# Optimization experiments

Hardware: AMD Instinct MI355X
Metric: run time of the kernel (lower is better)

Reference implementation:

```python
import jax, jax.numpy as jnp
import numpy as np

N_NODES, N_EDGES, N_GRAPHS, N_LOCS = 50000, 800000, 64, 50
HEADS, OUT_PER_HEAD = 3, 43            # ceil(128/3) = 43
MID = HEADS * OUT_PER_HEAD             # 129
GAT_HIDDEN, MLP_HIDDEN = 128, 256
NEG_SLOPE = 0.2


def _leaky(v):
    return jnp.where(v > 0, v, NEG_SLOPE * v)


def _gat_layer(h_in, src, dst, W, a_src, a_dst, b, concat):
    """PyG GATConv: per-edge attention, segment softmax over dst, scatter-add."""
    N = h_in.shape[0]
    H, O = a_src.shape
    h = (h_in @ W).reshape(N, H, O)                      # [N,H,O]
    es = jnp.einsum('nho,ho->nh', h, a_src)              # alpha_src per node
    ed = jnp.einsum('nho,ho->nh', h, a_dst)              # alpha_dst per node
    e = _leaky(es[src] + ed[dst])                        # [E,H]
    m = jax.ops.segment_max(e, dst, num_segments=N)
    m = jnp.where(jnp.isfinite(m), m, 0.0)
    w = jnp.exp(e - m[dst])
    z = jax.ops.segment_sum(w, dst, num_segments=N)
    alpha = w / (z[dst] + 1e-16)                         # softmax over in-edges of dst
    out = jax.ops.segment_sum(h[src] * alpha[:, :, None], dst, num_segments=N)
    out = out.reshape(N, H * O) if concat else out.mean(axis=1)
    return out + b


def setup_inputs() -> dict:
    key = jax.random.key(0)
    ks = jax.random.split(key, 20)
    x = jax.random.normal(ks[0], (N_NODES, 6), jnp.float32)
    edge_index = jax.random.randint(ks[1], (2, N_EDGES), 0, N_NODES)
    batch = jnp.sort(jax.random.randint(ks[2], (N_NODES,), 0, N_GRAPHS))
    loc = jax.random.uniform(ks[3], (N_GRAPHS, N_LOCS, 2), jnp.float32)

    def p(k, shape):
        return jax.random.normal(k, shape, jnp.float32) * 0.1

    return dict(
        x=x, loc=loc, edge_index=edge_index, batch=batch,
        W0=p(ks[4], (6, MID)), as0=p(ks[5], (HEADS, OUT_PER_HEAD)),
        ad0=p(ks[6], (HEADS, OUT_PER_HEAD)), b0=jnp.zeros((MID,), jnp.float32),
        W1=p(ks[7], (MID, MID)), as1=p(ks[8], (HEADS, OUT_PER_HEAD)),
        ad1=p(ks[9], (HEADS, OUT_PER_HEAD)), b1=jnp.zeros((MID,), jnp.float32),
        W2=p(ks[10], (MID, GAT_HIDDEN)), as2=p(ks[11], (1, GAT_HIDDEN)),
        ad2=p(ks[12], (1, GAT_HIDDEN)), b2=jnp.zeros((GAT_HIDDEN,), jnp.float32),
        Wl1=p(ks[13], (2, MLP_HIDDEN)), bl1=jnp.zeros((MLP_HIDDEN,), jnp.float32),
        Wl2=p(ks[14], (MLP_HIDDEN, GAT_HIDDEN)), bl2=jnp.zeros((GAT_HIDDEN,), jnp.float32),
    )


def reference(x, loc, W0, as0, ad0, b0, W1, as1, ad1, b1, W2, as2, ad2, b2,
              Wl1, bl1, Wl2, bl2, edge_index, batch):
    N = x.shape[0]
    loops = jnp.arange(N)                                # add_self_loops=True
    src = jnp.concatenate([edge_index[0], loops])
    dst = jnp.concatenate([edge_index[1], loops])

    h = _leaky(_gat_layer(x, src, dst, W0, as0, ad0, b0, True))
    h = _leaky(_gat_layer(h, src, dst, W1, as1, ad1, b1, True))
    h = _gat_layer(h, src, dst, W2, as2, ad2, b2, False)  # heads=1, concat=False

    # global_mean_pool over graphs
    sums = jax.ops.segment_sum(h, batch, num_segments=N_GRAPHS)
    cnt = jax.ops.segment_sum(jnp.ones((N, 1), h.dtype), batch, num_segments=N_GRAPHS)
    graph_emb = sums / jnp.maximum(cnt, 1.0)              # [B,128]

    # location encoder MLP + mean pool over locations
    loc_emb = jnp.tanh(loc @ Wl1 + bl1) @ Wl2 + bl2       # [B,L,128]
    loc_pooled = loc_emb.mean(axis=1)                     # [B,128]

    return jnp.concatenate([graph_emb, loc_pooled], axis=-1)  # [B,256]
```

## Files before the change

### kernel.cpp

```cpp
#include <hip/hip_runtime.h>
#include <hip/hip_bf16.h>
#include <math.h>

#define N_NODES  50000
#define N_EDGES  800000
#define E_TOT    850000
#define N_GRAPHS 64
#define N_LOCS   50
#define SCAN_B   ((N_NODES + 255) / 256)
#define TSTRIDE  128
#define HSTRIDE  132
#define ASTRIDE  160

#define EB_B     ((E_TOT + 255) / 256)
#define GEMM0_B  ((N_NODES + 31) / 32)
#define NPB3     85
#define RST3     136
#define ESED3_B  ((N_NODES + NPB3 - 1) / NPB3)
#define POOL_B   ((N_NODES + 31) / 32)

typedef __hip_bfloat16 bf16;
typedef __attribute__((ext_vector_type(8))) short bf16x8;
typedef __attribute__((ext_vector_type(4))) float f32x4;

__device__ int      g_deg[N_NODES];
__device__ int      g_rowptr[N_NODES + 1];
__device__ int      g_bsum[SCAN_B];
__device__ int      g_slot[E_TOT];
__device__ int      g_csrc[E_TOT];
__device__ float    g_Wp0[6 * 132];
__device__ __align__(256) unsigned short g_Tb[(size_t)N_NODES * TSTRIDE];
__device__ float    g_Te[N_NODES];
__device__ __align__(16) float g_H[(size_t)N_NODES * HSTRIDE];
__device__ __align__(16) unsigned short g_Ah[(size_t)N_NODES * ASTRIDE];
__device__ __align__(16) unsigned short g_Al[(size_t)N_NODES * ASTRIDE];
#define WQ1_N (5 * 9 * 64 * 8)
#define WQ2_N (5 * 8 * 64 * 8)
__device__ __align__(16) unsigned short g_Wq1h[WQ1_N], g_Wq1l[WQ1_N];
__device__ __align__(16) unsigned short g_Wq2h[WQ2_N], g_Wq2l[WQ2_N];
__device__ float    g_es[N_NODES * 3];
__device__ float    g_ed[N_NODES * 3];
__device__ unsigned g_gmk[9];
__device__ float    g_gsum[N_GRAPHS * 128];
__device__ float    g_gcnt[N_GRAPHS];

__device__ __forceinline__ float lrelu(float x){ return x > 0.f ? x : 0.2f * x; }
__device__ __forceinline__ int   clampi(int v, int lo, int hi){ return v < lo ? lo : (v > hi ? hi : v); }
__device__ __forceinline__ float finz(float v){
    unsigned u = __float_as_uint(v);
    return ((u & 0x7F800000u) == 0x7F800000u) ? 0.f : v;
}
__device__ __forceinline__ unsigned short f2bu(float x){
    union { bf16 b; unsigned short u; } cv; cv.b = __float2bfloat16(x); return cv.u;
}
__device__ __forceinline__ float bu2f(unsigned short u){ return __uint_as_float(((unsigned)u) << 16); }
__device__ __forceinline__ unsigned fkey(float f){
    unsigned u = __float_as_uint(f);
    return (u & 0x80000000u) ? ~u : (u | 0x80000000u);
}
__device__ __forceinline__ float kinv(unsigned k){
    return __uint_as_float((k & 0x80000000u) ? (k ^ 0x80000000u) : ~k);
}
__device__ __forceinline__ float expc(float a){ return __expf(fminf(fmaxf(a, -80.f), 0.f)); }
__device__ __forceinline__ void edge_sd(const int* ei, int e, int& src, int& dst){
    if (e < N_EDGES){
        src = clampi(ei[e], 0, N_NODES - 1);
        dst = clampi(ei[N_EDGES + e], 0, N_NODES - 1);
    } else {
        src = dst = e - N_EDGES;
    }
}
#define RL_I(v, i) __builtin_amdgcn_readlane((v), (i))
#define RL_F(v, i) __uint_as_float((unsigned)__builtin_amdgcn_readlane((int)__float_as_uint(v), (i)))

#define PRE_TOT (N_NODES + N_GRAPHS*128 + 9 + 6*132 + WQ1_N + WQ2_N)
__global__ void k_pre(const float* __restrict__ W0, const float* __restrict__ W1,
                      const float* __restrict__ W2){
    int i = blockIdx.x * blockDim.x + threadIdx.x;
    if (i < N_NODES){ g_deg[i] = 0; return; }
    i -= N_NODES;
    if (i < N_GRAPHS * 128){ g_gsum[i] = 0.f; return; }
    i -= N_GRAPHS * 128;
    if (i < 9){ g_gmk[i] = 0u; return; }
    i -= 9;
    if (i < 6 * 132){
        int k = i / 132, c = i - k * 132;
        g_Wp0[i] = (c < 129) ? finz(W0[k * 129 + c]) : 0.f;
        return;
    }
    i -= 6 * 132;
    if (i < WQ1_N){
        int kt = i / 4608;
        int r1 = i - kt * 4608;
        int nt = r1 / 512;
        int r2 = r1 - nt * 512;
        int ln = r2 >> 3, j = r2 & 7;
        int k = kt * 32 + (ln >> 4) * 8 + j;
        int c = nt * 16 + (ln & 15);
        float v = (k < 129 && c < 129) ? finz(W1[k * 129 + c]) : 0.f;
        unsigned short h = f2bu(v);
        g_Wq1h[i] = h;
        g_Wq1l[i] = f2bu(v - bu2f(h));
        return;
    }
    i -= WQ1_N;
    if (i < WQ2_N){
        int kt = i / 4096;
        int r1 = i - kt * 4096;
        int nt = r1 / 512;
        int r2 = r1 - nt * 512;
        int ln = r2 >> 3, j = r2 & 7;
        int k = kt * 32 + (ln >> 4) * 8 + j;
        int c = nt * 16 + (ln & 15);
        float v = (k < 129 && c < 128) ? finz(W2[k * 128 + c]) : 0.f;
        unsigned short h = f2bu(v);
        g_Wq2h[i] = h;
        g_Wq2l[i] = f2bu(v - bu2f(h));
    }
}

__global__ __launch_bounds__(256)
void k_g0deg(const float* __restrict__ X, const int* __restrict__ ei){
    if (blockIdx.x < EB_B){
        int e = blockIdx.x * 256 + threadIdx.x;
        if (e >= E_TOT) return;
        int src, dst; edge_sd(ei, e, src, dst);
        (void)src;
        g_slot[e] = atomicAdd(&g_deg[dst], 1);
        return;
    }
    const int R = 4, CO = 129;
    const float* Wp = g_Wp0;
    int bid = blockIdx.x - EB_B;
    int tid = threadIdx.x;
    int rg = tid >> 5;
    int g  = tid & 31;
    int n0 = bid * (8 * R) + rg * R;
    const float4* wp = (const float4*)Wp;
    float4 acc[R];
    float accE[R];
    #pragma unroll
    for (int r = 0; r < R; r++){ acc[r] = make_float4(0.f,0.f,0.f,0.f); accE[r] = 0.f; }

    const float* ar[R];
    #pragma unroll
    for (int r = 0; r < R; r++){
        int n = n0 + r;
        ar[r] = X + (size_t)(n < N_NODES ? n : N_NODES - 1) * 6;
    }
    #pragma unroll
    for (int k = 0; k < 6; k++){
        float4 w = wp[k * 33 + g];
        float we = (g == 0) ? Wp[k * 132 + 128] : 0.f;
        #pragma unroll
        for (int r = 0; r < R; r++){
            float a = ar[r][k];
            acc[r].x += a * w.x; acc[r].y += a * w.y;
            acc[r].z += a * w.z; acc[r].w += a * w.w;
            if (g == 0) accE[r] += a * we;
        }
    }

    #pragma unroll
    for (int r = 0; r < R; r++){
        int n = n0 + r;
        if (n >= N_NODES) break;
        unsigned* tw = (unsigned*)(g_Tb + (size_t)n * TSTRIDE);
        tw[g * 2]     = ((unsigned)f2bu(finz(acc[r].x)) ) | ((unsigned)f2bu(finz(acc[r].y)) << 16);
        tw[g * 2 + 1] = ((unsigned)f2bu(finz(acc[r].z)) ) | ((unsigned)f2bu(finz(acc[r].w)) << 16);
        if (CO > 128 && g == 0) g_Te[n] = finz(accE[r]);
    }
}

__global__ void k_scan1(){
    __shared__ int s[256];
    int i = blockIdx.x * 256 + threadIdx.x;
    int v = (i < N_NODES) ? g_deg[i] : 0;
    s[threadIdx.x] = v;
    __syncthreads();
    for (int off = 1; off < 256; off <<= 1){
        int add = (threadIdx.x >= off) ? s[threadIdx.x - off] : 0;
        __syncthreads();
        s[threadIdx.x] += add;
        __syncthreads();
    }
    if (threadIdx.x == 255) g_bsum[blockIdx.x] = s[255];
    if (i < N_NODES) g_rowptr[i] = s[threadIdx.x] - v;
}

__global__ __launch_bounds__(256)
void k_scan23(){
    __shared__ int red[256];
    int b = blockIdx.x, tid = threadIdx.x;
    red[tid] = (tid < b) ? g_bsum[tid] : 0;
    __syncthreads();
    #pragma unroll
    for (int off = 128; off >= 1; off >>= 1){
        if (tid < off) red[tid] += red[tid + off];
        __syncthreads();
    }
    int S = red[0];
    int i = b * 256 + tid;
    if (i < N_NODES) g_rowptr[i] += S;
    if (b == 0 && tid == 0) g_rowptr[N_NODES] = E_TOT;
}

__device__ __forceinline__ void esed3_body(const float* __restrict__ as,
                                           const float* __restrict__ ad,
                                           int base, int bid){
    __shared__ unsigned short rows[NPB3 * RST3];
    __shared__ unsigned sm[3];
    int tid = threadIdx.x;
    if (tid < 3) sm[tid] = 0u;
    int n0 = bid * NPB3;
    for (int ch = tid; ch < NPB3 * 16; ch += 256){
        int r = ch >> 4, k = ch & 15;
        int n = n0 + r; if (n >= N_NODES) n = N_NODES - 1;
        *(uint4*)&rows[r * RST3 + k * 8] =
            *(const uint4*)(g_Tb + (size_t)n * TSTRIDE + k * 8);
    }
    __syncthreads();
    int idx = n0 * 3 + tid;
    if (tid < NPB3 * 3 && idx < N_NODES * 3){
        int r = tid / 3, h = tid - r * 3;
        const unsigned short* rw = rows + r * RST3;
        float a = 0.f, b = 0.f;
        #pragma unroll 4
        for (int o = 0; o < 43; o++){
            int col = h * 43 + o;
            float v = (col < 128) ? bu2f(rw[col]) : finz(g_Te[n0 + r]);
            a += v * finz(as[h * 43 + o]);
            b += v * finz(ad[h * 43 + o]);
        }
        a = finz(a); b = finz(b);
        g_es[idx] = a; g_ed[idx] = b;
        atomicMax(&sm[h], fkey(a));
    }
    __syncthreads();
    if (tid < 3) atomicMax(&g_gmk[base + tid], sm[tid]);
}

__global__ __launch_bounds__(256)
void k_esed3(const float* __restrict__ as, const float* __restrict__ ad, int base){
    esed3_body(as, ad, base, blockIdx.x);
}

__global__ __launch_bounds__(256)
void k_esfill(const float* __restrict__ as, const float* __restrict__ ad,
              const int* __restrict__ ei){
    if (blockIdx.x < EB_B){
        int e = blockIdx.x * 256 + threadIdx.x;
        if (e >= E_TOT) return;
        int src, dst; edge_sd(ei, e, src, dst);
        int pos = clampi(g_rowptr[dst] + g_slot[e], 0, E_TOT - 1);
        g_csrc[pos] = src;
        return;
    }
    esed3_body(as, ad, 0, blockIdx.x - EB_B);
}

__global__ __launch_bounds__(256)
void k_esedR(const float* __restrict__ as, const float* __restrict__ ad, int base){
    __shared__ unsigned sm[1];
    int tid = threadIdx.x;
    if (tid == 0) sm[0] = 0u;
    __syncthreads();
    int n = blockIdx.x * 256 + tid;
    bool act = n < N_NODES;
    int nn = act ? n : N_NODES - 1;
    const uint4* rp = (const uint4*)(g_Tb + (size_t)nn * TSTRIDE);
    float a = 0.f, b = 0.f;
    #pragma unroll
    for (int k = 0; k < 16; k++){
        uint4 ch = rp[k];
        unsigned dw[4] = {ch.x, ch.y, ch.z, ch.w};
        #pragma unroll
        for (int j = 0; j < 4; j++){
            unsigned d = dw[j];
            int o = k * 8 + j * 2;
            float v0 = bu2f((unsigned short)(d & 0xFFFFu));
            float v1 = bu2f((unsigned short)(d >> 16));
            a += v0 * finz(as[o]);     b += v0 * finz(ad[o]);
            a += v1 * finz(as[o + 1]); b += v1 * finz(ad[o + 1]);
        }
    }
    if (act){
        a = finz(a); b = finz(b);
        g_es[n] = a; g_ed[n] = b;
        atomicMax(&sm[0], fkey(a));
    }
    __syncthreads();
    if (tid == 0) atomicMax(&g_gmk[base], sm[0]);
}

template<int NT, bool HASE>
__global__ __launch_bounds__(256, 3)
void k_gmm(){
    const unsigned short* Wh = HASE ? g_Wq1h : g_Wq2h;
    const unsigned short* Wl = HASE ? g_Wq1l : g_Wq2l;
    int lane = threadIdx.x & 63, wv = threadIdx.x >> 6;
    int row0 = blockIdx.x * 64 + wv * 16;
    int rl = row0 + (lane & 15);
    if (rl >= N_NODES) rl = N_NODES - 1;
    const bf16x8* Ah = (const bf16x8*)(g_Ah + (size_t)rl * ASTRIDE);
    const bf16x8* Al = (const bf16x8*)(g_Al + (size_t)rl * ASTRIDE);
    int ao = lane >> 4;

    f32x4 acc[NT] = {};
    #pragma unroll
    for (int kt = 0; kt < 5; kt++){
        bf16x8 ah = Ah[kt * 4 + ao];
        bf16x8 al = Al[kt * 4 + ao];
        const bf16x8* wh = (const bf16x8*)Wh + (size_t)(kt * NT) * 64 + lane;
        const bf16x8* wl = (const bf16x8*)Wl + (size_t)(kt * NT) * 64 + lane;
        #pragma unroll
        for (int t = 0; t < NT; t++){
            bf16x8 bh = wh[t * 64];
            bf16x8 bl = wl[t * 64];
            acc[t] = __builtin_amdgcn_mfma_f32_16x16x32_bf16(ah, bh, acc[t], 0, 0, 0);
            acc[t] = __builtin_amdgcn_mfma_f32_16x16x32_bf16(al, bh, acc[t], 0, 0, 0);
            acc[t] = __builtin_amdgcn_mfma_f32_16x16x32_bf16(ah, bl, acc[t], 0, 0, 0);
        }
    }

    int rq = row0 + (lane >> 4) * 4;
    int c  = lane & 15;
    #pragma unroll
    for (int t = 0; t < NT; t++){
        int col = t * 16 + c;
        #pragma unroll
        for (int q = 0; q < 4; q++){
            int rr = rq + q;
            if (rr >= N_NODES) continue;
            float v = finz(acc[t][q]);
            if (col < 128)            g_Tb[(size_t)rr * TSTRIDE + col] = f2bu(v);
            else if (HASE && col == 128) g_Te[rr] = v;
        }
    }
}

template<int H, int O, int C, bool LEAKY, bool WRITEA>
__global__ __launch_bounds__(256)
void k_fgat(const float* __restrict__ bias, int base){
    const int CH = 64 / H;
    __shared__ float lw[4][64];
    int wv = threadIdx.x >> 6, lane = threadIdx.x & 63;
    int n = blockIdx.x * 4 + wv;
    if (n >= N_NODES) return;
    int r0 = clampi(g_rowptr[n], 0, E_TOT);
    int r1 = clampi(g_rowptr[n + 1], r0, E_TOT);

    const int jmine = lane / H;
    const int hmine = lane - jmine * H;
    const float edm = finz(g_ed[n * H + hmine]);
    const float mxm = lrelu(finz(kinv(g_gmk[base + hmine])) + edm);
    const unsigned* tb = (const unsigned*)g_Tb;

    const int c0 = 2 * lane, c1 = 2 * lane + 1;
    const int h0 = c0 / O, h1 = c1 / O;
    float* lwp = lw[wv];

    float a0 = 0.f, a1 = 0.f, zA = 0.f, zB = 0.f, A2 = 0.f, z2 = 0.f;

#define EDGE(tt, pv, ss) { \
    float x0 = __uint_as_float((pv) << 16); \
    float x1 = __uint_as_float((pv) & 0xFFFF0000u); \
    float wA = lwp[(tt) * H + h0]; \
    a0 += wA * x0; zA += wA; \
    if (H > 1){ \
        float wB = lwp[(tt) * H + h1]; \
        a1 += wB * x1; zB += wB; \
    } else { \
        a1 += wA * x1; \
    } \
    if (C > 128){ \
        float w2 = lwp[(tt) * H + (H - 1)]; \
        float te = finz(g_Te[ss]); \
        A2 += w2 * te; z2 += w2; \
    } \
}

    for (int bse = r0; bse < r1; bse += CH){
        int m = r1 - bse; if (m > CH) m = CH;
        float w = 0.f; int sA = 0;
        if (jmine < m){
            sA = clampi(g_csrc[bse + jmine], 0, N_NODES - 1);
            w = expc(lrelu(finz(g_es[sA * H + hmine]) + edm) - mxm);
        }
        lwp[lane] = w;
        int t = 0;
        for (; t + 4 <= m; t += 4){
            int s0 = RL_I(sA, (t + 0) * H);
            int s1 = RL_I(sA, (t + 1) * H);
            int s2 = RL_I(sA, (t + 2) * H);
            int s3 = RL_I(sA, (t + 3) * H);
            unsigned pv0 = tb[(size_t)s0 * 64 + lane];
            unsigned pv1 = tb[(size_t)s1 * 64 + lane];
            unsigned pv2 = tb[(size_t)s2 * 64 + lane];
            unsigned pv3 = tb[(size_t)s3 * 64 + lane];
            EDGE(t + 0, pv0, s0)
            EDGE(t + 1, pv1, s1)
            EDGE(t + 2, pv2, s2)
            EDGE(t + 3, pv3, s3)
        }
        for (; t < m; ++t){
            int s0 = RL_I(sA, t * H);
            unsigned pv0 = tb[(size_t)s0 * 64 + lane];
            EDGE(t, pv0, s0)
        }
    }
#undef EDGE

    if (H == 1){ zB = zA; }

    float o0 = finz(a0 / (zA + 1e-16f)) + finz(bias[c0]);
    float o1 = finz(a1 / (zB + 1e-16f)) + finz(bias[c1]);
    if (LEAKY){ o0 = lrelu(o0); o1 = lrelu(o1); }
    o0 = finz(o0); o1 = finz(o1);
    float o2 = 0.f;
    if (C > 128){
        o2 = finz(A2 / (z2 + 1e-16f)) + finz(bias[128]);
        if (LEAKY) o2 = lrelu(o2);
        o2 = finz(o2);
    }

    if (WRITEA){
        unsigned short hh0 = f2bu(o0), hh1 = f2bu(o1);
        unsigned short ll0 = f2bu(o0 - bu2f(hh0)), ll1 = f2bu(o1 - bu2f(hh1));
        unsigned* ah = (unsigned*)(g_Ah + (size_t)n * ASTRIDE);
        unsigned* al = (unsigned*)(g_Al + (size_t)n * ASTRIDE);
        ah[lane] = (unsigned)hh0 | ((unsigned)hh1 << 16);
        al[lane] = (unsigned)ll0 | ((unsigned)ll1 << 16);
        if (lane < 16){
            unsigned ph = 0u, pl = 0u;
            if (C > 128 && lane == 0){
                unsigned short h2 = f2bu(o2);
                ph = (unsigned)h2;
                pl = (unsigned)f2bu(o2 - bu2f(h2));
            }
            ah[64 + lane] = ph;
            al[64 + lane] = pl;
        }
    } else {
        g_H[(size_t)n * HSTRIDE + c0] = o0;
        g_H[(size_t)n * HSTRIDE + c1] = o1;
        if (C > 128 && lane == 0) g_H[(size_t)n * HSTRIDE + 128] = o2;
    }
}

__global__ __launch_bounds__(256)
void k_poolloc(const int* __restrict__ batch, const float* __restrict__ loc,
               const float* __restrict__ Wl1, const float* __restrict__ bl1,
               const float* __restrict__ Wl2, const float* __restrict__ bl2,
               float* __restrict__ out){
    if (blockIdx.x < POOL_B){
        int c = threadIdx.x & 127;
        int n0 = blockIdx.x * 32 + (threadIdx.x >> 7) * 16;
        int bprev = -1; float acc = 0.f;
        for (int j = 0; j < 16; j++){
            int n = n0 + j;
            if (n >= N_NODES) break;
            int b = clampi(batch[n], 0, N_GRAPHS - 1);
            if (b != bprev){
                if (bprev >= 0) atomicAdd(&g_gsum[bprev * 128 + c], acc);
                acc = 0.f; bprev = b;
            }
            acc += finz(g_H[(size_t)n * HSTRIDE + c]);
        }
        if (bprev >= 0) atomicAdd(&g_gsum[bprev * 128 + c], acc);
        return;
    }
    int b = blockIdx.x - POOL_B, t = threadIdx.x;
    if (b == N_GRAPHS){
        if (t < N_GRAPHS){
            int lo = 0, hi = N_NODES;
            while (lo < hi){ int mid = (lo + hi) >> 1; if (batch[mid] <  t) lo = mid + 1; else hi = mid; }
            int start = lo;
            lo = 0; hi = N_NODES;
            while (lo < hi){ int mid = (lo + hi) >> 1; if (batch[mid] <= t) lo = mid + 1; else hi = mid; }
            g_gcnt[t] = (float)(lo - start);
        }
        return;
    }
    __shared__ float hs[256];
    float w0 = finz(Wl1[t]);
    float w1 = finz(Wl1[256 + t]);
    float bb = finz(bl1[t]);
    float s = 0.f;
    #pragma unroll 5
    for (int l = 0; l < N_LOCS; l++){
        float x0 = finz(loc[((size_t)b * N_LOCS + l) * 2]);
        float x1 = finz(loc[((size_t)b * N_LOCS + l) * 2 + 1]);
        s += tanhf(x0 * w0 + x1 * w1 + bb);
    }
    hs[t] = s;
    __syncthreads();
    if (t < 128){
        float acc = 0.f;
        #pragma unroll 8
        for (int j = 0; j < 256; j++) acc += hs[j] * finz(Wl2[(size_t)j * 128 + t]);
        out[(size_t)b * 256 + 128 + t] = finz(acc * (1.f / (float)N_LOCS) + finz(bl2[t]));
    }
}

__global__ void k_fin(float* __restrict__ out){
    int idx = blockIdx.x * blockDim.x + threadIdx.x;
    if (idx >= N_GRAPHS * 128) return;
    int b = idx >> 7, c = idx & 127;
    out[b * 256 + c] = finz(finz(g_gsum[idx]) / fmaxf(g_gcnt[b], 1.f));
}

extern "C" void kernel_launch(void* const* d_in, const int* in_sizes, int n_in,
                              void* d_out, int out_size, void* d_ws, size_t ws_size,
                              hipStream_t stream){
    static const int want[20] = {300000, 6400, 1600000, 50000,
                                 774, 129, 129, 129,
                                 16641, 129, 129, 129,
                                 16512, 128, 128, 128,
                                 512, 256, 32768, 128};
    const void* P[20];
    bool assigned[20];
    for (int s = 0; s < 20; s++){ P[s] = nullptr; assigned[s] = false; }
    bool ok = (n_in == 20);
    if (ok){
        for (int i = 0; i < 20; i++){
            int sz = in_sizes[i], hit = -1;
            for (int s = 0; s < 20; s++)
                if (!assigned[s] && want[s] == sz){ hit = s; break; }
            if (hit < 0){ ok = false; break; }
            P[hit] = d_in[i]; assigned[hit] = true;
        }
        for (int s = 0; s < 20 && ok; s++) if (!assigned[s]) ok = false;
    }
    if (!ok) for (int s = 0; s < 20 && s < n_in; s++) P[s] = d_in[s];

    const float* x    = (const float*)P[0];
    const float* loc  = (const float*)P[1];
    const int*   ei   = (const int*)  P[2];
    const int*   batch= (const int*)  P[3];
    const float* W0   = (const float*)P[4];
    const float* as0  = (const float*)P[5];
    const float* ad0  = (const float*)P[6];
    const float* b0   = (const float*)P[7];
    const float* W1   = (const float*)P[8];
    const float* as1  = (const float*)P[9];
    const float* ad1  = (const float*)P[10];
    const float* b1   = (const float*)P[11];
    const float* W2   = (const float*)P[12];
    const float* as2  = (const float*)P[13];
    const float* ad2  = (const float*)P[14];
    const float* b2   = (const float*)P[15];
    const float* Wl1  = (const float*)P[16];
    const float* bl1  = (const float*)P[17];
    const float* Wl2  = (const float*)P[18];
    const float* bl2  = (const float*)P[19];
    float* out = (float*)d_out;
    (void)d_ws; (void)ws_size; (void)out_size;

    const int MFMA_B  = (N_NODES + 63) / 64;
    const int GB = (N_NODES + 3) / 4;

    k_pre    <<<(PRE_TOT + 255) / 256, 256, 0, stream>>>(W0, W1, W2);
    k_g0deg  <<<EB_B + GEMM0_B, 256, 0, stream>>>(x, ei);
    k_scan1  <<<SCAN_B, 256, 0, stream>>>();
    k_scan23 <<<SCAN_B, 256, 0, stream>>>();
    k_esfill <<<EB_B + ESED3_B, 256, 0, stream>>>(as0, ad0, ei);

    k_fgat<3, 43, 129, true, true><<<GB, 256, 0, stream>>>(b0, 0);

    k_gmm<9, true><<<MFMA_B, 256, 0, stream>>>();
    k_esed3<<<ESED3_B, 256, 0, stream>>>(as1, ad1, 3);
    k_fgat<3, 43, 129, true, true><<<GB, 256, 0, stream>>>(b1, 3);

    k_gmm<8, false><<<MFMA_B, 256, 0, stream>>>();
    k_esedR<<<(N_NODES + 255) / 256, 256, 0, stream>>>(as2, ad2, 6);
    k_fgat<1, 128, 128, false, false><<<GB, 256, 0, stream>>>(b2, 6);

    k_poolloc<<<POOL_B + N_GRAPHS + 1, 256, 0, stream>>>(batch, loc, Wl1, bl1, Wl2, bl2, out);
    k_fin  <<<(N_GRAPHS * 128 + 255) / 256, 256, 0, stream>>>(out);
}
```

Measured before the change: 393.8 us.

## Merge scan kernels and trim per-edge softmax-denominator work in fused GAT

The two-kernel prefix scan over node degrees is replaced by a single kernel in which each block recomputes its own prefix by summing all earlier degrees directly. In the fused GAT aggregation, only one running denominator is kept per lane, and the other heads' denominators come from lane shuffles after the loop. The 129th channel is handled by lane 63, which reuses its head-2 weight. For the single-head layer, weights are read by register shuffle instead of shared memory. This saves one launch and per-edge LDS reads and adds, but block-prefix recomputation costs work that grows with block index.

```diff
diff --git a/kernel.cpp b/kernel.cpp
--- a/kernel.cpp
+++ b/kernel.cpp
@@ -25,7 +25,6 @@
 
 __device__ int      g_deg[N_NODES];
 __device__ int      g_rowptr[N_NODES + 1];
-__device__ int      g_bsum[SCAN_B];
 __device__ int      g_slot[E_TOT];
 __device__ int      g_csrc[E_TOT];
 __device__ float    g_Wp0[6 * 132];
@@ -172,36 +171,32 @@
     }
 }
 
-__global__ void k_scan1(){
+__global__ __launch_bounds__(256)
+void k_scan(){
+    __shared__ int rs[256];
     __shared__ int s[256];
-    int i = blockIdx.x * 256 + threadIdx.x;
+    int b = blockIdx.x, tid = threadIdx.x;
+    int pre = 0;
+    for (int i = tid; i < b * 256; i += 256) pre += g_deg[i];
+    rs[tid] = pre;
+    __syncthreads();
+    #pragma unroll
+    for (int off = 128; off >= 1; off >>= 1){
+        if (tid < off) rs[tid] += rs[tid + off];
+        __syncthreads();
+    }
+    int base = rs[0];
+    int i = b * 256 + tid;
     int v = (i < N_NODES) ? g_deg[i] : 0;
-    s[threadIdx.x] = v;
+    s[tid] = v;
     __syncthreads();
     for (int off = 1; off < 256; off <<= 1){
-        int add = (threadIdx.x >= off) ? s[threadIdx.x - off] : 0;
+        int add = (tid >= off) ? s[tid - off] : 0;
         __syncthreads();
-        s[threadIdx.x] += add;
+        s[tid] += add;
         __syncthreads();
     }
-    if (threadIdx.x == 255) g_bsum[blockIdx.x] = s[255];
-    if (i < N_NODES) g_rowptr[i] = s[threadIdx.x] - v;
-}
-
-__global__ __launch_bounds__(256)
-void k_scan23(){
-    __shared__ int red[256];
-    int b = blockIdx.x, tid = threadIdx.x;
-    red[tid] = (tid < b) ? g_bsum[tid] : 0;
-    __syncthreads();
-    #pragma unroll
-    for (int off = 128; off >= 1; off >>= 1){
-        if (tid < off) red[tid] += red[tid + off];
-        __syncthreads();
-    }
-    int S = red[0];
-    int i = b * 256 + tid;
-    if (i < N_NODES) g_rowptr[i] += S;
+    if (i < N_NODES) g_rowptr[i] = base + s[tid] - v;
     if (b == 0 && tid == 0) g_rowptr[N_NODES] = E_TOT;
 }
 
@@ -360,23 +355,21 @@
     const int h0 = c0 / O, h1 = c1 / O;
     float* lwp = lw[wv];
 
-    float a0 = 0.f, a1 = 0.f, zA = 0.f, zB = 0.f, A2 = 0.f, z2 = 0.f;
+    float a0 = 0.f, a1 = 0.f, zA = 0.f, A2 = 0.f;
 
 #define EDGE(tt, pv, ss) { \
     float x0 = __uint_as_float((pv) << 16); \
     float x1 = __uint_as_float((pv) & 0xFFFF0000u); \
-    float wA = lwp[(tt) * H + h0]; \
-    a0 += wA * x0; zA += wA; \
     if (H > 1){ \
+        float wA = lwp[(tt) * H + h0]; \
         float wB = lwp[(tt) * H + h1]; \
-        a1 += wB * x1; zB += wB; \
+        a0 += wA * x0; zA += wA; \
+        a1 += wB * x1; \
+        if (C > 128){ float te = finz(g_Te[ss]); A2 += wB * te; } \
     } else { \
+        float wA = RL_F(w, (tt)); \
+        a0 += wA * x0; zA += wA; \
         a1 += wA * x1; \
-    } \
-    if (C > 128){ \
-        float w2 = lwp[(tt) * H + (H - 1)]; \
-        float te = finz(g_Te[ss]); \
-        A2 += w2 * te; z2 += w2; \
     } \
 }
 
@@ -387,7 +380,7 @@
             sA = clampi(g_csrc[bse + jmine], 0, N_NODES - 1);
             w = expc(lrelu(finz(g_es[sA * H + hmine]) + edm) - mxm);
         }
-        lwp[lane] = w;
+        if (H > 1) lwp[lane] = w;
         int t = 0;
         for (; t + 4 <= m; t += 4){
             int s0 = RL_I(sA, (t + 0) * H);
@@ -411,7 +404,15 @@
     }
 #undef EDGE
 
-    if (H == 1){ zB = zA; }
+    float zB;
+    if (H == 1){
+        zB = zA;
+    } else {
+        float sz0 = RL_F(zA, 0);
+        float sz1 = RL_F(zA, 22);
+        float sz2 = RL_F(zA, 43);
+        zB = (h1 == 0) ? sz0 : ((h1 == 1) ? sz1 : sz2);
+    }
 
     float o0 = finz(a0 / (zA + 1e-16f)) + finz(bias[c0]);
     float o1 = finz(a1 / (zB + 1e-16f)) + finz(bias[c1]);
@@ -419,7 +420,7 @@
     o0 = finz(o0); o1 = finz(o1);
     float o2 = 0.f;
     if (C > 128){
-        o2 = finz(A2 / (z2 + 1e-16f)) + finz(bias[128]);
+        o2 = finz(A2 / (zB + 1e-16f)) + finz(bias[128]);
         if (LEAKY) o2 = lrelu(o2);
         o2 = finz(o2);
     }
@@ -431,20 +432,20 @@
         unsigned* al = (unsigned*)(g_Al + (size_t)n * ASTRIDE);
         ah[lane] = (unsigned)hh0 | ((unsigned)hh1 << 16);
         al[lane] = (unsigned)ll0 | ((unsigned)ll1 << 16);
-        if (lane < 16){
-            unsigned ph = 0u, pl = 0u;
-            if (C > 128 && lane == 0){
+        if (lane >= 1 && lane < 16){ ah[64 + lane] = 0u; al[64 + lane] = 0u; }
+        if (C > 128){
+            if (lane == 63){
                 unsigned short h2 = f2bu(o2);
-                ph = (unsigned)h2;
-                pl = (unsigned)f2bu(o2 - bu2f(h2));
+                ah[64] = (unsigned)h2;
+                al[64] = (unsigned)f2bu(o2 - bu2f(h2));
             }
-            ah[64 + lane] = ph;
-            al[64 + lane] = pl;
+        } else if (lane == 0){
+            ah[64] = 0u; al[64] = 0u;
         }
     } else {
         g_H[(size_t)n * HSTRIDE + c0] = o0;
         g_H[(size_t)n * HSTRIDE + c1] = o1;
-        if (C > 128 && lane == 0) g_H[(size_t)n * HSTRIDE + 128] = o2;
+        if (C > 128 && lane == 63) g_H[(size_t)n * HSTRIDE + 128] = o2;
     }
 }
 
@@ -562,8 +563,7 @@
 
     k_pre    <<<(PRE_TOT + 255) / 256, 256, 0, stream>>>(W0, W1, W2);
     k_g0deg  <<<EB_B + GEMM0_B, 256, 0, stream>>>(x, ei);
-    k_scan1  <<<SCAN_B, 256, 0, stream>>>();
-    k_scan23 <<<SCAN_B, 256, 0, stream>>>();
+    k_scan   <<<SCAN_B, 256, 0, stream>>>();
     k_esfill <<<EB_B + ESED3_B, 256, 0, stream>>>(as0, ad0, ei);
 
     k_fgat<3, 43, 129, true, true><<<GB, 256, 0, stream>>>(b0, 0);
```

After: 420.7 us. +6.8%, slower.
